# Kernel optimization log

Measured on AMD Instinct MI355X. Metric: run time of the kernel, lower is better.

The kernel has to match this reference:

```python
import jax, jax.numpy as jnp
import numpy as np

NUM_CLASSES = 80
D_IMG = 2048
D_WORD = 300
D_MID = 1024
B = 8
CONV = 14


def setup_inputs() -> dict:
    key = jax.random.key(0)
    ks = jax.random.split(key, 6)
    s = lambda k, shape, sc: jax.random.normal(k, shape, dtype=jnp.float32) * sc
    return {
        "batch_size": B,
        "img_feature_map": jax.random.normal(ks[0], (B, D_IMG, CONV, CONV), dtype=jnp.float32),
        "word_features": jax.random.normal(ks[1], (NUM_CLASSES, D_WORD), dtype=jnp.float32),
        "W1": s(ks[2], (D_MID, D_IMG), 0.02),
        "W2": s(ks[3], (D_MID, D_WORD), 0.02),
        "W3": s(ks[4], (D_MID, D_MID), 0.02),
        "b3": jnp.zeros((D_MID,), jnp.float32),
        "Wa": s(ks[5], (1, D_MID), 0.02),
        "ba": jnp.zeros((1,), jnp.float32),
    }


def reference(batch_size, img_feature_map, word_features, W1, W2, W3, b3, Wa, ba):
    # img_feature_map: [B, D_img, H, W] -> [B, H, W, D_img] (matches torch double transpose)
    Bn, D, H, W = img_feature_map.shape
    fmap = jnp.transpose(img_feature_map, (0, 2, 3, 1))                 # [B,H,W,D]
    f_wh = jnp.einsum('bhwd,md->bhwm', fmap, W1)                        # fc_1: [B,H,W,M]
    f_wd = word_features @ W2.T                                         # fc_2: [C,M]
    # broadcast multiply (no explicit repeat) + tanh
    t = jnp.tanh(f_wh[:, :, :, None, :] * f_wd)                         # [B,H,W,C,M]
    lb = jnp.einsum('bhwcm,nm->bhwcn', t, W3) + b3                      # fc_3: [B,H,W,C,M]
    coef = jnp.einsum('bhwcm,m->bhwc', lb, Wa[0]) + ba[0]               # fc_a: [B,H,W,C]
    # softmax over spatial positions per (batch, class)
    C = coef.shape[-1]
    coef = jax.nn.softmax(coef.reshape(Bn, H * W, C), axis=1).reshape(Bn, H, W, C)
    # softmax-weighted spatial pooling -> [B, C, D]
    return jnp.einsum('bhwc,bhwd->bcd', coef, fmap)
```

## Files before the change

kernel.cpp:

```cpp
#include <hip/hip_runtime.h>
#include <hip/hip_bf16.h>
#include <stdint.h>

#define NB 8
#define DIMG 2048
#define HWN 196
#define PN 1568
#define PPAD 1600
#define DMID 1024
#define NC 80
#define DWORD 300
#define PART 16

typedef short bf16x8 __attribute__((ext_vector_type(8)));
typedef float f32x4 __attribute__((ext_vector_type(4)));

__device__ __forceinline__ unsigned short f2bf(float x) {
  union { float f; unsigned u; } c; c.f = x;
  unsigned r = c.u + 0x7FFFu + ((c.u >> 16) & 1u);
  return (unsigned short)(r >> 16);
}

__global__ void k_tc(const float* __restrict__ img, unsigned short* __restrict__ fmapH,
                     const float* __restrict__ W1, unsigned short* __restrict__ W1h) {
  __shared__ float tile[32][33];
  int bx = blockIdx.x;
  int tx = threadIdx.x, ty = threadIdx.y;
  if (bx < 3584) {
    int d0 = (bx & 63) * 32;
    int rem = bx >> 6;
    int h0 = (rem % 7) * 32, b = rem / 7;
    const float* src = img + (size_t)b * DIMG * HWN;
#pragma unroll
    for (int i = 0; i < 32; i += 8) {
      int hw = h0 + tx;
      tile[ty + i][tx] = (hw < HWN) ? src[(size_t)(d0 + ty + i) * HWN + hw] : 0.f;
    }
    __syncthreads();
#pragma unroll
    for (int i = 0; i < 32; i += 8) {
      int hw = h0 + ty + i;
      if (hw < HWN)
        fmapH[(size_t)(b * HWN + hw) * DIMG + d0 + tx] = f2bf(tile[tx][ty + i]);
    }
  } else {
    int tid = ty * 32 + tx;
    int i = ((bx - 3584) * 256 + tid) * 4;
    f32x4 v = *(const f32x4*)(W1 + i);
    ushort4 s;
    s.x = f2bf(v[0]); s.y = f2bf(v[1]); s.z = f2bf(v[2]); s.w = f2bf(v[3]);
    *(ushort4*)(W1h + i) = s;
  }
}

__global__ __launch_bounds__(256) void k_fwdweff(const float* __restrict__ word,
                                                 const float* __restrict__ W2,
                                                 float* __restrict__ fwd,
                                                 const float* __restrict__ Wa,
                                                 const float* __restrict__ W3,
                                                 float* __restrict__ partial) {
  __shared__ __align__(16) float w2s[64 * DWORD];
  __shared__ __align__(16) float wds[16 * DWORD];
  int bx = blockIdx.x, t = threadIdx.x;
  if (bx < 80) {
    int m0 = (bx & 15) * 64, c0 = (bx >> 4) * 16;
    const float SC = 2.8853900817779268f;
    for (int u = t; u < 64 * 75; u += 256) {
      int r = u / 75, q = u - r * 75;
      *(f32x4*)&w2s[r * DWORD + q * 4] =
          *(const f32x4*)(W2 + (size_t)(m0 + r) * DWORD + q * 4);
    }
    for (int u = t; u < 16 * 75; u += 256) {
      int r = u / 75, q = u - r * 75;
      f32x4 v = *(const f32x4*)(word + (size_t)(c0 + r) * DWORD + q * 4);
      *(f32x4*)&wds[r * DWORD + q * 4] = v * SC;
    }
    __syncthreads();
    int ci = t >> 4, mi = t & 15;
    f32x4 a0 = {0.f, 0.f, 0.f, 0.f}, a1 = a0, a2 = a0, a3 = a0;
    const float* wr = &wds[ci * DWORD];
    for (int q = 0; q < 75; ++q) {
      f32x4 wv = *(const f32x4*)&wr[q * 4];
      f32x4 b0 = *(const f32x4*)&w2s[(mi)*DWORD + q * 4];
      f32x4 b1 = *(const f32x4*)&w2s[(mi + 16) * DWORD + q * 4];
      f32x4 b2 = *(const f32x4*)&w2s[(mi + 32) * DWORD + q * 4];
      f32x4 b3 = *(const f32x4*)&w2s[(mi + 48) * DWORD + q * 4];
#pragma unroll
      for (int u = 0; u < 4; ++u) {
        a0[u] = fmaf(wv[u], b0[u], a0[u]);
        a1[u] = fmaf(wv[u], b1[u], a1[u]);
        a2[u] = fmaf(wv[u], b2[u], a2[u]);
        a3[u] = fmaf(wv[u], b3[u], a3[u]);
      }
    }
    float* dst = fwd + (size_t)(c0 + ci) * DMID + m0 + mi;
    dst[0]  = a0[0] + a0[1] + a0[2] + a0[3];
    dst[16] = a1[0] + a1[1] + a1[2] + a1[3];
    dst[32] = a2[0] + a2[1] + a2[2] + a2[3];
    dst[48] = a3[0] + a3[1] + a3[2] + a3[3];
  } else {
    int idx = bx - 80;
    int m = (idx & 3) * 256 + t;
    int n0 = (idx >> 2) * 64;
    float acc = 0.f;
    for (int n = n0; n < n0 + 64; ++n) acc = fmaf(Wa[n], W3[(size_t)n * DMID + m], acc);
    partial[(size_t)(idx >> 2) * DMID + m] = acc;
  }
}

#define GLDS(g, l) \
  __builtin_amdgcn_global_load_lds((const __attribute__((address_space(1))) void*)(g), \
                                   (__attribute__((address_space(3))) void*)(l), 16, 0, 0)

__global__ __launch_bounds__(256) void k_fused(const unsigned short* __restrict__ A,
                                               const unsigned short* __restrict__ Bw,
                                               const float* __restrict__ fwd,
                                               const float* __restrict__ partial,
                                               float* __restrict__ coefp) {
  __shared__ __align__(16) char smem[36864];
  unsigned short* As = (unsigned short*)smem;
  unsigned short* Bs = As + 3 * 2048;
  float* Xl = (float*)smem;
  float* bl = Xl + 32 * 68;
  float* wl = bl + 80 * 68;
  int p0 = blockIdx.x * 32, mz = blockIdx.y;
  int n0 = mz * 64;
  int t = threadIdx.x;
  int w = t >> 6, l = t & 63;
  f32x4 zero = {0.f, 0.f, 0.f, 0.f};
  f32x4 acc0 = zero, acc1 = zero;

  int r0 = t >> 3, cch = t & 7;
  int r1 = r0 + 32;
  const unsigned short* ga0 = A + (size_t)(p0 + r0) * 2048 + ((cch ^ (r0 & 7)) << 3);
  const unsigned short* gb0 = Bw + (size_t)(n0 + r0) * 2048 + ((cch ^ (r0 & 7)) << 3);
  const unsigned short* gb1 = Bw + (size_t)(n0 + r1) * 2048 + ((cch ^ (r1 & 7)) << 3);

  int ra = l & 15;
  int rb = w * 16 + (l & 15);
  int cc = l >> 4;
  int a_k0 = ra * 64 + (((cc) ^ (ra & 7)) << 3);
  int a_k1 = ra * 64 + (((cc + 4) ^ (ra & 7)) << 3);
  int b_k0 = rb * 64 + (((cc) ^ (rb & 7)) << 3);
  int b_k1 = rb * 64 + (((cc + 4) ^ (rb & 7)) << 3);

#define STAGE(bi, kk) do { \
    GLDS(ga0 + (kk), As + (bi) * 2048 + t * 8); \
    GLDS(gb0 + (kk), Bs + (bi) * 4096 + t * 8); \
    GLDS(gb1 + (kk), Bs + (bi) * 4096 + t * 8 + 2048); \
  } while (0)

#define COMPUTE(bi) do { \
    const unsigned short* ap = As + (bi) * 2048; \
    const unsigned short* bp = Bs + (bi) * 4096; \
    bf16x8 A0 = *(const bf16x8*)(ap + a_k0); \
    bf16x8 A1 = *(const bf16x8*)(ap + a_k0 + 1024); \
    bf16x8 B0 = *(const bf16x8*)(bp + b_k0); \
    __builtin_amdgcn_s_setprio(1); \
    acc0 = __builtin_amdgcn_mfma_f32_16x16x32_bf16(A0, B0, acc0, 0, 0, 0); \
    acc1 = __builtin_amdgcn_mfma_f32_16x16x32_bf16(A1, B0, acc1, 0, 0, 0); \
    __builtin_amdgcn_s_setprio(0); \
    bf16x8 A2 = *(const bf16x8*)(ap + a_k1); \
    bf16x8 A3 = *(const bf16x8*)(ap + a_k1 + 1024); \
    bf16x8 B1 = *(const bf16x8*)(bp + b_k1); \
    __builtin_amdgcn_s_setprio(1); \
    acc0 = __builtin_amdgcn_mfma_f32_16x16x32_bf16(A2, B1, acc0, 0, 0, 0); \
    acc1 = __builtin_amdgcn_mfma_f32_16x16x32_bf16(A3, B1, acc1, 0, 0, 0); \
    __builtin_amdgcn_s_setprio(0); \
  } while (0)

  STAGE(0, 0);
  STAGE(1, 64);
  asm volatile("s_waitcnt vmcnt(3)" ::: "memory");
  __builtin_amdgcn_s_barrier();
  __builtin_amdgcn_sched_barrier(0);
  for (int kt = 0; kt < 32; ++kt) {
    int cur = kt % 3;
    if (kt < 30) STAGE((kt + 2) % 3, (kt + 2) * 64);
    COMPUTE(cur);
    if (kt < 30) {
      asm volatile("s_waitcnt vmcnt(3)" ::: "memory");
      __builtin_amdgcn_s_barrier();
      __builtin_amdgcn_sched_barrier(0);
    } else if (kt == 30) {
      asm volatile("s_waitcnt vmcnt(0)" ::: "memory");
      __builtin_amdgcn_s_barrier();
      __builtin_amdgcn_sched_barrier(0);
    }
  }
  __syncthreads();

  {
    int xr = (l >> 4) << 2, xc = w * 16 + (l & 15);
#pragma unroll
    for (int q = 0; q < 4; ++q) {
      Xl[(xr + q) * 68 + xc]        = acc0[q];
      Xl[(xr + q + 16) * 68 + xc]   = acc1[q];
    }
#pragma unroll
    for (int i = 0; i < 5; ++i) {
      int idx = t + 256 * i;
      int r = idx >> 4, c4 = (idx & 15) << 2;
      *(f32x4*)&bl[r * 68 + c4] = *(const f32x4*)(fwd + (size_t)r * DMID + n0 + c4);
    }
    if (t < 64) {
      float v = 0.f;
#pragma unroll
      for (int s = 0; s < 16; ++s) v += partial[(size_t)s * DMID + n0 + t];
      wl[t] = -2.f * v;
    }
  }
  __syncthreads();

  int pi = t >> 4, ci = t & 15;
  float acc[2][5];
#pragma unroll
  for (int j = 0; j < 2; ++j)
#pragma unroll
    for (int k = 0; k < 5; ++k) acc[j][k] = 0.f;

#pragma unroll 1
  for (int mm = 0; mm < 64; mm += 4) {
    f32x4 wv = *(const f32x4*)&wl[mm];
    f32x4 av0 = *(const f32x4*)&Xl[(pi)*68 + mm];
    f32x4 av1 = *(const f32x4*)&Xl[(pi + 16) * 68 + mm];
#pragma unroll
    for (int k = 0; k < 5; ++k) {
      f32x4 bv = *(const f32x4*)&bl[(k * 16 + ci) * 68 + mm];
#pragma unroll
      for (int u = 0; u < 4; ++u) {
        float wgt = wv[u], b = bv[u];
        float e0 = __builtin_amdgcn_exp2f(av0[u] * b);
        float e1 = __builtin_amdgcn_exp2f(av1[u] * b);
        acc[0][k] = fmaf(wgt, __builtin_amdgcn_rcpf(1.f + e0), acc[0][k]);
        acc[1][k] = fmaf(wgt, __builtin_amdgcn_rcpf(1.f + e1), acc[1][k]);
      }
    }
  }
  float* cp = coefp + (size_t)mz * (PN * NC);
#pragma unroll
  for (int j = 0; j < 2; ++j) {
    int p = p0 + pi + 16 * j;
    if (p < PN) {
#pragma unroll
      for (int k = 0; k < 5; ++k)
        cp[(size_t)p * NC + k * 16 + ci] = acc[j][k];
    }
  }
#undef STAGE
#undef COMPUTE
}

__global__ __launch_bounds__(256) void k_pool(const float* __restrict__ coefp,
                                              const float* __restrict__ img,
                                              float* __restrict__ out) {
  __shared__ __align__(16) float wt[HWN][16];
  __shared__ float red[16][16];
  __shared__ float mxs[16], inv[16];
  int dc = blockIdx.x * 256, cg = blockIdx.y * 16, b = blockIdx.z;
  int t = threadIdx.x;
  for (int i = t; i < HWN * 4; i += 256) {
    int hw = i >> 2, j4 = (i & 3) << 2;
    size_t o = (size_t)(b * HWN + hw) * NC + cg + j4;
    f32x4 s = {0.f, 0.f, 0.f, 0.f};
#pragma unroll
    for (int z = 0; z < PART; ++z) s += *(const f32x4*)&coefp[o + (size_t)z * (PN * NC)];
    *(f32x4*)&wt[hw][j4] = s;
  }
  __syncthreads();
  int j = t & 15, g = t >> 4;
  float pm = -1e30f;
  for (int hw = g; hw < HWN; hw += 16) pm = fmaxf(pm, wt[hw][j]);
  red[g][j] = pm;
  __syncthreads();
  if (t < 16) {
    float m = red[0][t];
#pragma unroll
    for (int g2 = 1; g2 < 16; ++g2) m = fmaxf(m, red[g2][t]);
    mxs[t] = m;
  }
  __syncthreads();
  float mj = mxs[j], ps = 0.f;
  for (int hw = g; hw < HWN; hw += 16) {
    float e = __builtin_amdgcn_exp2f((wt[hw][j] - mj) * 1.4426950408889634f);
    wt[hw][j] = e;
    ps += e;
  }
  red[g][j] = ps;
  __syncthreads();
  if (t < 16) {
    float s = 0.f;
#pragma unroll
    for (int g2 = 0; g2 < 16; ++g2) s += red[g2][t];
    inv[t] = 1.f / s;
  }
  __syncthreads();
  float acc[16];
#pragma unroll
  for (int q = 0; q < 16; ++q) acc[q] = 0.f;
  const float* fpd = img + ((size_t)b * DIMG + dc + t) * HWN;
  for (int hw = 0; hw < HWN; ++hw) {
    float v = fpd[hw];
#pragma unroll
    for (int q = 0; q < 16; ++q) acc[q] = fmaf(wt[hw][q], v, acc[q]);
  }
#pragma unroll
  for (int q = 0; q < 16; ++q)
    out[((size_t)b * NC + cg + q) * DIMG + dc + t] = acc[q] * inv[q];
}

extern "C" void kernel_launch(void* const* d_in, const int* in_sizes, int n_in,
                              void* d_out, int out_size, void* d_ws, size_t ws_size,
                              hipStream_t stream) {
  const float* img  = (const float*)d_in[1];
  const float* word = (const float*)d_in[2];
  const float* W1   = (const float*)d_in[3];
  const float* W2   = (const float*)d_in[4];
  const float* W3   = (const float*)d_in[5];
  const float* Wa   = (const float*)d_in[7];
  float* out = (float*)d_out;
  char* ws = (char*)d_ws;

  unsigned short* fmapH   = (unsigned short*)(ws + 0);
  unsigned short* W1h     = (unsigned short*)(ws + 6553600);
  float*          fwd     = (float*)(ws + 10747904);
  float*          partial = (float*)(ws + 11141120);
  float*          coefp   = (float*)(ws + 11206656);

  hipLaunchKernelGGL(k_tc, dim3(5632), dim3(32, 8), 0, stream, img, fmapH, W1, W1h);
  hipLaunchKernelGGL(k_fwdweff, dim3(144), dim3(256), 0, stream,
                     word, W2, fwd, Wa, W3, partial);
  hipLaunchKernelGGL(k_fused, dim3(50, 16), dim3(256), 0, stream,
                     fmapH, W1h, fwd, partial, coefp);
  hipLaunchKernelGGL(k_pool, dim3(8, 5, 8), dim3(256), 0, stream, coefp, img, out);
  (void)in_sizes; (void)n_in; (void)out_size; (void)ws_size;
}
```

Before: 111.0 us.

## Process two M-tiles per block, overlapping sigmoid math with the second GEMM

```diff
diff --git a/kernel.cpp b/kernel.cpp
--- a/kernel.cpp
+++ b/kernel.cpp
@@ -10,7 +10,7 @@
 #define DMID 1024
 #define NC 80
 #define DWORD 300
-#define PART 16
+#define PART 8
 
 typedef short bf16x8 __attribute__((ext_vector_type(8)));
 typedef float f32x4 __attribute__((ext_vector_type(4)));
@@ -19,6 +19,12 @@
   union { float f; unsigned u; } c; c.f = x;
   unsigned r = c.u + 0x7FFFu + ((c.u >> 16) & 1u);
   return (unsigned short)(r >> 16);
+}
+__device__ __forceinline__ float bflo(unsigned u) {
+  union { unsigned v; float f; } c; c.v = u << 16; return c.f;
+}
+__device__ __forceinline__ float bfhi(unsigned u) {
+  union { unsigned v; float f; } c; c.v = u & 0xffff0000u; return c.f;
 }
 
 __global__ void k_tc(const float* __restrict__ img, unsigned short* __restrict__ fmapH,
@@ -117,24 +123,42 @@
                                                const float* __restrict__ fwd,
                                                const float* __restrict__ partial,
                                                float* __restrict__ coefp) {
-  __shared__ __align__(16) char smem[36864];
+  __shared__ __align__(16) char smem[76544];
   unsigned short* As = (unsigned short*)smem;
   unsigned short* Bs = As + 3 * 2048;
-  float* Xl = (float*)smem;
-  float* bl = Xl + 32 * 68;
-  float* wl = bl + 80 * 68;
-  int p0 = blockIdx.x * 32, mz = blockIdx.y;
-  int n0 = mz * 64;
+  float* Xl0 = (float*)(smem + 36864);
+  float* Xl1 = (float*)(smem + 45568);
+  unsigned short* bl = (unsigned short*)(smem + 54272);
+  float* wl = (float*)(smem + 76032);
+  int p0 = blockIdx.x * 32;
+  int n0 = blockIdx.y * 128;
   int t = threadIdx.x;
   int w = t >> 6, l = t & 63;
-  f32x4 zero = {0.f, 0.f, 0.f, 0.f};
-  f32x4 acc0 = zero, acc1 = zero;
+  int pi = t >> 4, ci = t & 15;
+
+#pragma unroll
+  for (int i = 0; i < 10; ++i) {
+    int g = t + 256 * i;
+    int row = g >> 5, c4 = (g & 31) << 2;
+    f32x4 v = *(const f32x4*)(fwd + (size_t)row * DMID + n0 + c4);
+    ushort4 h;
+    h.x = f2bf(v[0]); h.y = f2bf(v[1]); h.z = f2bf(v[2]); h.w = f2bf(v[3]);
+    *(ushort4*)&bl[row * 136 + c4] = h;
+  }
+  if (t < 128) {
+    float v = 0.f;
+#pragma unroll
+    for (int s = 0; s < 16; ++s) v += partial[(size_t)s * DMID + n0 + t];
+    wl[t] = -2.f * v;
+  }
 
   int r0 = t >> 3, cch = t & 7;
   int r1 = r0 + 32;
-  const unsigned short* ga0 = A + (size_t)(p0 + r0) * 2048 + ((cch ^ (r0 & 7)) << 3);
-  const unsigned short* gb0 = Bw + (size_t)(n0 + r0) * 2048 + ((cch ^ (r0 & 7)) << 3);
-  const unsigned short* gb1 = Bw + (size_t)(n0 + r1) * 2048 + ((cch ^ (r1 & 7)) << 3);
+  const unsigned short* gA   = A  + (size_t)(p0 + r0) * 2048 + ((cch ^ (r0 & 7)) << 3);
+  const unsigned short* gB0a = Bw + (size_t)(n0 + r0) * 2048 + ((cch ^ (r0 & 7)) << 3);
+  const unsigned short* gB1a = Bw + (size_t)(n0 + r1) * 2048 + ((cch ^ (r1 & 7)) << 3);
+  const unsigned short* gB0b = gB0a + 64 * 2048;
+  const unsigned short* gB1b = gB1a + 64 * 2048;
 
   int ra = l & 15;
   int rb = w * 16 + (l & 15);
@@ -144,40 +168,69 @@
   int b_k0 = rb * 64 + (((cc) ^ (rb & 7)) << 3);
   int b_k1 = rb * 64 + (((cc + 4) ^ (rb & 7)) << 3);
 
-#define STAGE(bi, kk) do { \
-    GLDS(ga0 + (kk), As + (bi) * 2048 + t * 8); \
-    GLDS(gb0 + (kk), Bs + (bi) * 4096 + t * 8); \
-    GLDS(gb1 + (kk), Bs + (bi) * 4096 + t * 8 + 2048); \
+#define STAGEA(bi, kk) do { \
+    GLDS(gA + (kk), As + (bi) * 2048 + t * 8); \
+    GLDS(gB0a + (kk), Bs + (bi) * 4096 + t * 8); \
+    GLDS(gB1a + (kk), Bs + (bi) * 4096 + t * 8 + 2048); \
   } while (0)
-
-#define COMPUTE(bi) do { \
+#define STAGEB(bi, kk) do { \
+    GLDS(gA + (kk), As + (bi) * 2048 + t * 8); \
+    GLDS(gB0b + (kk), Bs + (bi) * 4096 + t * 8); \
+    GLDS(gB1b + (kk), Bs + (bi) * 4096 + t * 8 + 2048); \
+  } while (0)
+#define COMPUTE(bi, c0v, c1v) do { \
     const unsigned short* ap = As + (bi) * 2048; \
     const unsigned short* bp = Bs + (bi) * 4096; \
     bf16x8 A0 = *(const bf16x8*)(ap + a_k0); \
     bf16x8 A1 = *(const bf16x8*)(ap + a_k0 + 1024); \
     bf16x8 B0 = *(const bf16x8*)(bp + b_k0); \
     __builtin_amdgcn_s_setprio(1); \
-    acc0 = __builtin_amdgcn_mfma_f32_16x16x32_bf16(A0, B0, acc0, 0, 0, 0); \
-    acc1 = __builtin_amdgcn_mfma_f32_16x16x32_bf16(A1, B0, acc1, 0, 0, 0); \
+    c0v = __builtin_amdgcn_mfma_f32_16x16x32_bf16(A0, B0, c0v, 0, 0, 0); \
+    c1v = __builtin_amdgcn_mfma_f32_16x16x32_bf16(A1, B0, c1v, 0, 0, 0); \
     __builtin_amdgcn_s_setprio(0); \
     bf16x8 A2 = *(const bf16x8*)(ap + a_k1); \
     bf16x8 A3 = *(const bf16x8*)(ap + a_k1 + 1024); \
     bf16x8 B1 = *(const bf16x8*)(bp + b_k1); \
     __builtin_amdgcn_s_setprio(1); \
-    acc0 = __builtin_amdgcn_mfma_f32_16x16x32_bf16(A2, B1, acc0, 0, 0, 0); \
-    acc1 = __builtin_amdgcn_mfma_f32_16x16x32_bf16(A3, B1, acc1, 0, 0, 0); \
+    c0v = __builtin_amdgcn_mfma_f32_16x16x32_bf16(A2, B1, c0v, 0, 0, 0); \
+    c1v = __builtin_amdgcn_mfma_f32_16x16x32_bf16(A3, B1, c1v, 0, 0, 0); \
     __builtin_amdgcn_s_setprio(0); \
   } while (0)
-
-  STAGE(0, 0);
-  STAGE(1, 64);
-  asm volatile("s_waitcnt vmcnt(3)" ::: "memory");
-  __builtin_amdgcn_s_barrier();
-  __builtin_amdgcn_sched_barrier(0);
+#define SIG2(XP, mcol, moff) do { \
+    int m_ = (mcol); \
+    float wg0 = wl[(moff) + m_], wg1 = wl[(moff) + m_ + 1]; \
+    float a00 = XP[pi * 68 + m_],        a01 = XP[pi * 68 + m_ + 1]; \
+    float a10 = XP[(pi + 16) * 68 + m_], a11 = XP[(pi + 16) * 68 + m_ + 1]; \
+    _Pragma("unroll") \
+    for (int k_ = 0; k_ < 5; ++k_) { \
+      unsigned bb = *(const unsigned*)&bl[(k_ * 16 + ci) * 136 + (moff) + m_]; \
+      float b0 = bflo(bb), b1 = bfhi(bb); \
+      float e00 = __builtin_amdgcn_exp2f(a00 * b0); \
+      float e01 = __builtin_amdgcn_exp2f(a01 * b1); \
+      float e10 = __builtin_amdgcn_exp2f(a10 * b0); \
+      float e11 = __builtin_amdgcn_exp2f(a11 * b1); \
+      sacc[0][k_] = fmaf(wg0, __builtin_amdgcn_rcpf(1.f + e00), sacc[0][k_]); \
+      sacc[0][k_] = fmaf(wg1, __builtin_amdgcn_rcpf(1.f + e01), sacc[0][k_]); \
+      sacc[1][k_] = fmaf(wg0, __builtin_amdgcn_rcpf(1.f + e10), sacc[1][k_]); \
+      sacc[1][k_] = fmaf(wg1, __builtin_amdgcn_rcpf(1.f + e11), sacc[1][k_]); \
+    } \
+  } while (0)
+
+  float sacc[2][5];
+#pragma unroll
+  for (int j = 0; j < 2; ++j)
+#pragma unroll
+    for (int k = 0; k < 5; ++k) sacc[j][k] = 0.f;
+
+  f32x4 zero = {0.f, 0.f, 0.f, 0.f};
+  f32x4 acc0 = zero, acc1 = zero;
+
+  STAGEA(0, 0);
+  STAGEA(1, 64);
+  __syncthreads();
   for (int kt = 0; kt < 32; ++kt) {
-    int cur = kt % 3;
-    if (kt < 30) STAGE((kt + 2) % 3, (kt + 2) * 64);
-    COMPUTE(cur);
+    if (kt < 30) STAGEA((kt + 2) % 3, (kt + 2) * 64);
+    COMPUTE(kt % 3, acc0, acc1);
     if (kt < 30) {
       asm volatile("s_waitcnt vmcnt(3)" ::: "memory");
       __builtin_amdgcn_s_barrier();
@@ -188,67 +241,63 @@
       __builtin_amdgcn_sched_barrier(0);
     }
   }
-  __syncthreads();
-
   {
     int xr = (l >> 4) << 2, xc = w * 16 + (l & 15);
 #pragma unroll
     for (int q = 0; q < 4; ++q) {
-      Xl[(xr + q) * 68 + xc]        = acc0[q];
-      Xl[(xr + q + 16) * 68 + xc]   = acc1[q];
-    }
-#pragma unroll
-    for (int i = 0; i < 5; ++i) {
-      int idx = t + 256 * i;
-      int r = idx >> 4, c4 = (idx & 15) << 2;
-      *(f32x4*)&bl[r * 68 + c4] = *(const f32x4*)(fwd + (size_t)r * DMID + n0 + c4);
-    }
-    if (t < 64) {
-      float v = 0.f;
-#pragma unroll
-      for (int s = 0; s < 16; ++s) v += partial[(size_t)s * DMID + n0 + t];
-      wl[t] = -2.f * v;
-    }
-  }
-  __syncthreads();
-
-  int pi = t >> 4, ci = t & 15;
-  float acc[2][5];
-#pragma unroll
-  for (int j = 0; j < 2; ++j)
-#pragma unroll
-    for (int k = 0; k < 5; ++k) acc[j][k] = 0.f;
+      Xl0[(xr + q) * 68 + xc]      = acc0[q];
+      Xl0[(xr + q + 16) * 68 + xc] = acc1[q];
+    }
+  }
+  __syncthreads();
+
+  acc0 = zero; acc1 = zero;
+  STAGEB(0, 0);
+  STAGEB(1, 64);
+  asm volatile("s_waitcnt vmcnt(3)" ::: "memory");
+  __builtin_amdgcn_s_barrier();
+  __builtin_amdgcn_sched_barrier(0);
+  for (int kt = 0; kt < 32; ++kt) {
+    if (kt < 30) STAGEB((kt + 2) % 3, (kt + 2) * 64);
+    COMPUTE(kt % 3, acc0, acc1);
+    SIG2(Xl0, 2 * kt, 0);
+    if (kt < 30) {
+      asm volatile("s_waitcnt vmcnt(3)" ::: "memory");
+      __builtin_amdgcn_s_barrier();
+      __builtin_amdgcn_sched_barrier(0);
+    } else if (kt == 30) {
+      asm volatile("s_waitcnt vmcnt(0)" ::: "memory");
+      __builtin_amdgcn_s_barrier();
+      __builtin_amdgcn_sched_barrier(0);
+    }
+  }
+  {
+    int xr = (l >> 4) << 2, xc = w * 16 + (l & 15);
+#pragma unroll
+    for (int q = 0; q < 4; ++q) {
+      Xl1[(xr + q) * 68 + xc]      = acc0[q];
+      Xl1[(xr + q + 16) * 68 + xc] = acc1[q];
+    }
+  }
+  __syncthreads();
 
 #pragma unroll 1
-  for (int mm = 0; mm < 64; mm += 4) {
-    f32x4 wv = *(const f32x4*)&wl[mm];
-    f32x4 av0 = *(const f32x4*)&Xl[(pi)*68 + mm];
-    f32x4 av1 = *(const f32x4*)&Xl[(pi + 16) * 68 + mm];
-#pragma unroll
-    for (int k = 0; k < 5; ++k) {
-      f32x4 bv = *(const f32x4*)&bl[(k * 16 + ci) * 68 + mm];
-#pragma unroll
-      for (int u = 0; u < 4; ++u) {
-        float wgt = wv[u], b = bv[u];
-        float e0 = __builtin_amdgcn_exp2f(av0[u] * b);
-        float e1 = __builtin_amdgcn_exp2f(av1[u] * b);
-        acc[0][k] = fmaf(wgt, __builtin_amdgcn_rcpf(1.f + e0), acc[0][k]);
-        acc[1][k] = fmaf(wgt, __builtin_amdgcn_rcpf(1.f + e1), acc[1][k]);
-      }
-    }
-  }
-  float* cp = coefp + (size_t)mz * (PN * NC);
+  for (int mm = 0; mm < 64; mm += 2) SIG2(Xl1, mm, 64);
+
+  float* cp = coefp + (size_t)blockIdx.y * (PN * NC);
 #pragma unroll
   for (int j = 0; j < 2; ++j) {
     int p = p0 + pi + 16 * j;
     if (p < PN) {
 #pragma unroll
       for (int k = 0; k < 5; ++k)
-        cp[(size_t)p * NC + k * 16 + ci] = acc[j][k];
-    }
-  }
-#undef STAGE
+        cp[(size_t)p * NC + k * 16 + ci] = sacc[j][k];
+    }
+  }
+#undef STAGEA
+#undef STAGEB
 #undef COMPUTE
+#undef SIG2
 }
 
 __global__ __launch_bounds__(256) void k_pool(const float* __restrict__ coefp,
@@ -330,7 +379,7 @@
   hipLaunchKernelGGL(k_tc, dim3(5632), dim3(32, 8), 0, stream, img, fmapH, W1, W1h);
   hipLaunchKernelGGL(k_fwdweff, dim3(144), dim3(256), 0, stream,
                      word, W2, fwd, Wa, W3, partial);
-  hipLaunchKernelGGL(k_fused, dim3(50, 16), dim3(256), 0, stream,
+  hipLaunchKernelGGL(k_fused, dim3(50, 8), dim3(256), 0, stream,
                      fmapH, W1h, fwd, partial, coefp);
   hipLaunchKernelGGL(k_pool, dim3(8, 5, 8), dim3(256), 0, stream, coefp, img, out);
   (void)in_sizes; (void)n_in; (void)out_size; (void)ws_size;
```

After: 116.1 us. +4.6%, slower.

## Warp-specialize fused kernel so MFMA GEMM overlaps tanh-attention epilogue

Applied to the files above, without the earlier changes.

```diff
diff --git a/kernel.cpp b/kernel.cpp
--- a/kernel.cpp
+++ b/kernel.cpp
@@ -6,11 +6,10 @@
 #define DIMG 2048
 #define HWN 196
 #define PN 1568
-#define PPAD 1600
 #define DMID 1024
 #define NC 80
 #define DWORD 300
-#define PART 16
+#define PART 4
 
 typedef short bf16x8 __attribute__((ext_vector_type(8)));
 typedef float f32x4 __attribute__((ext_vector_type(4)));
@@ -19,6 +18,12 @@
   union { float f; unsigned u; } c; c.f = x;
   unsigned r = c.u + 0x7FFFu + ((c.u >> 16) & 1u);
   return (unsigned short)(r >> 16);
+}
+__device__ __forceinline__ float bflo(unsigned u) {
+  union { unsigned v; float f; } c; c.v = u << 16; return c.f;
+}
+__device__ __forceinline__ float bfhi(unsigned u) {
+  union { unsigned v; float f; } c; c.v = u & 0xffff0000u; return c.f;
 }
 
 __global__ void k_tc(const float* __restrict__ img, unsigned short* __restrict__ fmapH,
@@ -112,143 +117,143 @@
   __builtin_amdgcn_global_load_lds((const __attribute__((address_space(1))) void*)(g), \
                                    (__attribute__((address_space(3))) void*)(l), 16, 0, 0)
 
-__global__ __launch_bounds__(256) void k_fused(const unsigned short* __restrict__ A,
+__global__ __launch_bounds__(512) void k_fused(const unsigned short* __restrict__ A,
                                                const unsigned short* __restrict__ Bw,
                                                const float* __restrict__ fwd,
                                                const float* __restrict__ partial,
                                                float* __restrict__ coefp) {
-  __shared__ __align__(16) char smem[36864];
+  __shared__ __align__(16) char smem[77568];
   unsigned short* As = (unsigned short*)smem;
-  unsigned short* Bs = As + 3 * 2048;
-  float* Xl = (float*)smem;
-  float* bl = Xl + 32 * 68;
-  float* wl = bl + 80 * 68;
-  int p0 = blockIdx.x * 32, mz = blockIdx.y;
-  int n0 = mz * 64;
+  unsigned short* Bs = (unsigned short*)(smem + 6144);
+  unsigned short* X0 = (unsigned short*)(smem + 30720);
+  unsigned short* X1 = (unsigned short*)(smem + 32832);
+  unsigned short* bl = (unsigned short*)(smem + 34944);
+  float*          wl = (float*)(smem + 76544);
+
+  int p0 = blockIdx.x * 16, mg = blockIdx.y;
   int t = threadIdx.x;
-  int w = t >> 6, l = t & 63;
-  f32x4 zero = {0.f, 0.f, 0.f, 0.f};
-  f32x4 acc0 = zero, acc1 = zero;
-
-  int r0 = t >> 3, cch = t & 7;
-  int r1 = r0 + 32;
-  const unsigned short* ga0 = A + (size_t)(p0 + r0) * 2048 + ((cch ^ (r0 & 7)) << 3);
-  const unsigned short* gb0 = Bw + (size_t)(n0 + r0) * 2048 + ((cch ^ (r0 & 7)) << 3);
-  const unsigned short* gb1 = Bw + (size_t)(n0 + r1) * 2048 + ((cch ^ (r1 & 7)) << 3);
-
+  int wid = t >> 6, l = t & 63;
+
+  int aq = t & 127;
+  int ar = aq >> 3, ac = aq & 7;
+  const unsigned short* gA = A + (size_t)(p0 + ar) * 2048 + ((ac ^ (ar & 7)) << 3);
+  int br = t >> 3, bc = t & 7;
+  const unsigned short* gB0 = Bw + (size_t)(mg * 256 + br) * 2048 + ((bc ^ (br & 7)) << 3);
+  const unsigned short* gB1 = Bw + (size_t)(mg * 256 + br + 32) * 2048 + ((bc ^ ((br + 32) & 7)) << 3);
   int ra = l & 15;
-  int rb = w * 16 + (l & 15);
+  int rb = wid * 16 + (l & 15);
   int cc = l >> 4;
   int a_k0 = ra * 64 + (((cc) ^ (ra & 7)) << 3);
   int a_k1 = ra * 64 + (((cc + 4) ^ (ra & 7)) << 3);
   int b_k0 = rb * 64 + (((cc) ^ (rb & 7)) << 3);
   int b_k1 = rb * 64 + (((cc + 4) ^ (rb & 7)) << 3);
 
-#define STAGE(bi, kk) do { \
-    GLDS(ga0 + (kk), As + (bi) * 2048 + t * 8); \
-    GLDS(gb0 + (kk), Bs + (bi) * 4096 + t * 8); \
-    GLDS(gb1 + (kk), Bs + (bi) * 4096 + t * 8 + 2048); \
+#define STAGE(bi, tile) do { \
+    int ch_ = (tile) >> 5, kk_ = ((tile) & 31) * 64; \
+    GLDS(gA + kk_, As + (bi) * 1024 + (t & 127) * 8); \
+    GLDS(gB0 + (size_t)ch_ * 64 * 2048 + kk_, Bs + (bi) * 4096 + t * 8); \
+    GLDS(gB1 + (size_t)ch_ * 64 * 2048 + kk_, Bs + (bi) * 4096 + t * 8 + 2048); \
   } while (0)
-
 #define COMPUTE(bi) do { \
-    const unsigned short* ap = As + (bi) * 2048; \
+    const unsigned short* ap = As + (bi) * 1024; \
     const unsigned short* bp = Bs + (bi) * 4096; \
     bf16x8 A0 = *(const bf16x8*)(ap + a_k0); \
-    bf16x8 A1 = *(const bf16x8*)(ap + a_k0 + 1024); \
     bf16x8 B0 = *(const bf16x8*)(bp + b_k0); \
-    __builtin_amdgcn_s_setprio(1); \
-    acc0 = __builtin_amdgcn_mfma_f32_16x16x32_bf16(A0, B0, acc0, 0, 0, 0); \
-    acc1 = __builtin_amdgcn_mfma_f32_16x16x32_bf16(A1, B0, acc1, 0, 0, 0); \
-    __builtin_amdgcn_s_setprio(0); \
+    acc = __builtin_amdgcn_mfma_f32_16x16x32_bf16(A0, B0, acc, 0, 0, 0); \
     bf16x8 A2 = *(const bf16x8*)(ap + a_k1); \
-    bf16x8 A3 = *(const bf16x8*)(ap + a_k1 + 1024); \
     bf16x8 B1 = *(const bf16x8*)(bp + b_k1); \
-    __builtin_amdgcn_s_setprio(1); \
-    acc0 = __builtin_amdgcn_mfma_f32_16x16x32_bf16(A2, B1, acc0, 0, 0, 0); \
-    acc1 = __builtin_amdgcn_mfma_f32_16x16x32_bf16(A3, B1, acc1, 0, 0, 0); \
-    __builtin_amdgcn_s_setprio(0); \
+    acc = __builtin_amdgcn_mfma_f32_16x16x32_bf16(A2, B1, acc, 0, 0, 0); \
   } while (0)
-
-  STAGE(0, 0);
-  STAGE(1, 64);
-  asm volatile("s_waitcnt vmcnt(3)" ::: "memory");
-  __builtin_amdgcn_s_barrier();
-  __builtin_amdgcn_sched_barrier(0);
-  for (int kt = 0; kt < 32; ++kt) {
-    int cur = kt % 3;
-    if (kt < 30) STAGE((kt + 2) % 3, (kt + 2) * 64);
-    COMPUTE(cur);
-    if (kt < 30) {
-      asm volatile("s_waitcnt vmcnt(3)" ::: "memory");
-      __builtin_amdgcn_s_barrier();
-      __builtin_amdgcn_sched_barrier(0);
-    } else if (kt == 30) {
-      asm volatile("s_waitcnt vmcnt(0)" ::: "memory");
-      __builtin_amdgcn_s_barrier();
-      __builtin_amdgcn_sched_barrier(0);
-    }
-  }
-  __syncthreads();
-
-  {
-    int xr = (l >> 4) << 2, xc = w * 16 + (l & 15);
-#pragma unroll
-    for (int q = 0; q < 4; ++q) {
-      Xl[(xr + q) * 68 + xc]        = acc0[q];
-      Xl[(xr + q + 16) * 68 + xc]   = acc1[q];
-    }
-#pragma unroll
-    for (int i = 0; i < 5; ++i) {
-      int idx = t + 256 * i;
-      int r = idx >> 4, c4 = (idx & 15) << 2;
-      *(f32x4*)&bl[r * 68 + c4] = *(const f32x4*)(fwd + (size_t)r * DMID + n0 + c4);
-    }
-    if (t < 64) {
-      float v = 0.f;
-#pragma unroll
-      for (int s = 0; s < 16; ++s) v += partial[(size_t)s * DMID + n0 + t];
-      wl[t] = -2.f * v;
-    }
-  }
-  __syncthreads();
-
-  int pi = t >> 4, ci = t & 15;
-  float acc[2][5];
-#pragma unroll
-  for (int j = 0; j < 2; ++j)
-#pragma unroll
-    for (int k = 0; k < 5; ++k) acc[j][k] = 0.f;
-
+#define XW(c) do { \
+    unsigned short* Xp_ = ((c) & 1) ? X1 : X0; \
+    int xr_ = (l >> 4) << 2, xc_ = wid * 16 + (l & 15); \
+    _Pragma("unroll") \
+    for (int q_ = 0; q_ < 4; ++q_) Xp_[(xr_ + q_) * 66 + xc_] = f2bf(acc[q_]); \
+  } while (0)
+
+  f32x4 acc = {0.f, 0.f, 0.f, 0.f};
+  float sacc[5] = {0.f, 0.f, 0.f, 0.f, 0.f};
+  int tc = t - 256;
+  int pi = tc >> 4, ci = tc & 15;
+
+  if (wid < 4) { STAGE(0, 0); STAGE(1, 1); }
+  __syncthreads();
+
+  for (int s = 0; s <= 128; ++s) {
+    if (wid < 4) {
+      if (s < 128) {
+        if (s && !(s & 31)) { XW((s >> 5) - 1); acc[0]=0.f; acc[1]=0.f; acc[2]=0.f; acc[3]=0.f; }
+        if (s < 126) STAGE((s + 2) % 3, s + 2);
+        COMPUTE(s % 3);
+        if (s < 126) { asm volatile("s_waitcnt vmcnt(3)" ::: "memory"); }
+        else         { asm volatile("s_waitcnt vmcnt(0)" ::: "memory"); }
+        if (!(s & 31)) { asm volatile("s_waitcnt lgkmcnt(0)" ::: "memory"); }
+      } else {
+        XW(3);
+        asm volatile("s_waitcnt lgkmcnt(0)" ::: "memory");
+      }
+    } else {
+      if (s < 20) {
+        int g = s * 256 + tc;
+        int row = g >> 6, mq = (g & 63) << 2;
+        f32x4 v = *(const f32x4*)(fwd + (size_t)row * DMID + mg * 256 + mq);
+        ushort4 h;
+        h.x = f2bf(v[0]); h.y = f2bf(v[1]); h.z = f2bf(v[2]); h.w = f2bf(v[3]);
+        *(ushort4*)&bl[row * 260 + mq] = h;
+      } else if (s == 20) {
+        float v = 0.f;
+#pragma unroll
+        for (int s16 = 0; s16 < 16; ++s16) v += partial[(size_t)s16 * DMID + mg * 256 + tc];
+        wl[tc] = -2.f * v;
+      }
+      if (s == 32) { asm volatile("s_waitcnt lgkmcnt(0)" ::: "memory"); }
+      int gs = s - 33;
+      if (gs >= 0 && gs < 96) {
+        int ch = gs >> 5, k = gs & 31;
+        const unsigned short* Xp = (ch & 1) ? X1 : X0;
+        int moff = ch << 6;
+        unsigned xa = *(const unsigned*)&Xp[pi * 66 + 2 * k];
+        float a0 = bflo(xa), a1 = bfhi(xa);
+        float wg0 = wl[moff + 2 * k], wg1 = wl[moff + 2 * k + 1];
+#pragma unroll
+        for (int kc = 0; kc < 5; ++kc) {
+          unsigned bb = *(const unsigned*)&bl[(kc * 16 + ci) * 260 + moff + 2 * k];
+          float b0 = bflo(bb), b1 = bfhi(bb);
+          float e0 = __builtin_amdgcn_exp2f(a0 * b0);
+          float e1 = __builtin_amdgcn_exp2f(a1 * b1);
+          sacc[kc] = fmaf(wg0, __builtin_amdgcn_rcpf(1.f + e0), sacc[kc]);
+          sacc[kc] = fmaf(wg1, __builtin_amdgcn_rcpf(1.f + e1), sacc[kc]);
+        }
+      }
+    }
+    __builtin_amdgcn_s_barrier();
+    __builtin_amdgcn_sched_barrier(0);
+  }
+
+  if (wid >= 4) {
 #pragma unroll 1
-  for (int mm = 0; mm < 64; mm += 4) {
-    f32x4 wv = *(const f32x4*)&wl[mm];
-    f32x4 av0 = *(const f32x4*)&Xl[(pi)*68 + mm];
-    f32x4 av1 = *(const f32x4*)&Xl[(pi + 16) * 68 + mm];
-#pragma unroll
-    for (int k = 0; k < 5; ++k) {
-      f32x4 bv = *(const f32x4*)&bl[(k * 16 + ci) * 68 + mm];
-#pragma unroll
-      for (int u = 0; u < 4; ++u) {
-        float wgt = wv[u], b = bv[u];
-        float e0 = __builtin_amdgcn_exp2f(av0[u] * b);
-        float e1 = __builtin_amdgcn_exp2f(av1[u] * b);
-        acc[0][k] = fmaf(wgt, __builtin_amdgcn_rcpf(1.f + e0), acc[0][k]);
-        acc[1][k] = fmaf(wgt, __builtin_amdgcn_rcpf(1.f + e1), acc[1][k]);
-      }
-    }
-  }
-  float* cp = coefp + (size_t)mz * (PN * NC);
-#pragma unroll
-  for (int j = 0; j < 2; ++j) {
-    int p = p0 + pi + 16 * j;
-    if (p < PN) {
-#pragma unroll
-      for (int k = 0; k < 5; ++k)
-        cp[(size_t)p * NC + k * 16 + ci] = acc[j][k];
-    }
+    for (int k = 0; k < 32; ++k) {
+      unsigned xa = *(const unsigned*)&X1[pi * 66 + 2 * k];
+      float a0 = bflo(xa), a1 = bfhi(xa);
+      float wg0 = wl[192 + 2 * k], wg1 = wl[192 + 2 * k + 1];
+#pragma unroll
+      for (int kc = 0; kc < 5; ++kc) {
+        unsigned bb = *(const unsigned*)&bl[(kc * 16 + ci) * 260 + 192 + 2 * k];
+        float b0 = bflo(bb), b1 = bfhi(bb);
+        float e0 = __builtin_amdgcn_exp2f(a0 * b0);
+        float e1 = __builtin_amdgcn_exp2f(a1 * b1);
+        sacc[kc] = fmaf(wg0, __builtin_amdgcn_rcpf(1.f + e0), sacc[kc]);
+        sacc[kc] = fmaf(wg1, __builtin_amdgcn_rcpf(1.f + e1), sacc[kc]);
+      }
+    }
+    float* cp = coefp + (size_t)mg * (PN * NC);
+#pragma unroll
+    for (int kc = 0; kc < 5; ++kc)
+      cp[(size_t)(p0 + pi) * NC + kc * 16 + ci] = sacc[kc];
   }
 #undef STAGE
 #undef COMPUTE
+#undef XW
 }
 
 __global__ __launch_bounds__(256) void k_pool(const float* __restrict__ coefp,
@@ -330,7 +335,7 @@
   hipLaunchKernelGGL(k_tc, dim3(5632), dim3(32, 8), 0, stream, img, fmapH, W1, W1h);
   hipLaunchKernelGGL(k_fwdweff, dim3(144), dim3(256), 0, stream,
                      word, W2, fwd, Wa, W3, partial);
-  hipLaunchKernelGGL(k_fused, dim3(50, 16), dim3(256), 0, stream,
+  hipLaunchKernelGGL(k_fused, dim3(98, 4), dim3(512), 0, stream,
                      fmapH, W1h, fwd, partial, coefp);
   hipLaunchKernelGGL(k_pool, dim3(8, 5, 8), dim3(256), 0, stream, coefp, img, out);
   (void)in_sizes; (void)n_in; (void)out_size; (void)ws_size;
```

After: 140.0 us. 26.1% more time.
